# Optimization experiments

Measured on AMD Instinct MI355X. Metric: run time of the kernel, lower is better.

## Reference

```python
import jax, jax.numpy as jnp
import numpy as np

# Module constants (from init_kwargs)
X_RANGE = (-10.0, 10.0)
Y_RANGE = (-10.0, 10.0)
N_X = 64
N_Y = 64
B = 16
N_CTX = 1024


def make_grid():
    # x counted forward, y counted backwards (image-row convention):
    # grid[k*N_X + j] = (xs[j], ys[k]) with ys from max to min.
    xs = jnp.linspace(X_RANGE[0], X_RANGE[1], N_X, dtype=jnp.float32)
    ys = jnp.linspace(Y_RANGE[1], Y_RANGE[0], N_Y, dtype=jnp.float32)
    gx, gy = jnp.meshgrid(xs, ys)          # each (N_Y, N_X)
    return jnp.stack([gx, gy], axis=-1).reshape(-1, 2)  # (G, 2)


def setup_inputs() -> dict:
    key = jax.random.key(0)
    k1, k2 = jax.random.split(key)
    X = jax.random.uniform(k1, (B, N_CTX, 2), dtype=jnp.float32,
                           minval=X_RANGE[0], maxval=X_RANGE[1])
    Y = jax.random.normal(k2, (B, N_CTX, 2), dtype=jnp.float32)
    log_l_scale = jnp.zeros((), dtype=jnp.float32)  # log(1.0)
    return {"X": X, "Y": Y, "log_l_scale": log_l_scale}


def reference(X, Y, log_l_scale):
    grid = make_grid()                                  # (G, 2)
    l = jnp.exp(log_l_scale)
    # squared distances via expansion to avoid a (B,G,n,2) intermediate
    g2 = jnp.sum(grid * grid, axis=-1)                  # (G,)
    x2 = jnp.sum(X * X, axis=-1)                        # (B, n)
    gx = jnp.einsum('gd,bnd->bgn', grid, X)             # (B, G, n)
    d2 = g2[None, :, None] + x2[:, None, :] - 2.0 * gx  # (B, G, n)
    Gram = jnp.exp(-0.5 * d2 / (l * l))                 # RBF kernel, B=1
    # expand Y with a leading ones (density) channel
    ones = jnp.ones(Y.shape[:2] + (1,), dtype=Y.dtype)
    EY = jnp.concatenate([ones, Y], axis=-1)            # (B, n, 3)
    FM = jnp.einsum('bgn,bnc->bgc', Gram, EY)           # (B, G, 3)
    dens = FM[..., 0:1]
    FM = jnp.concatenate([dens, FM[..., 1:] / dens], axis=-1)
    # (B, G, 3) -> (B, 3, N_Y, N_X)
    return FM.reshape(X.shape[0], N_Y, N_X, 3).transpose(0, 3, 1, 2)
```

## Files before the change

### kernel.cpp

```cpp
#include <hip/hip_runtime.h>
#include <hip/hip_bf16.h>
#include <math.h>


#define NB    16
#define NCTX  1024
#define NG    4096
#define NQ    4
#define NPQ   (NCTX / NQ)
#define CELLS 256

__global__ __launch_bounds__(1024, 1)
void ee_single(const float* __restrict__ X,
               const float* __restrict__ Y,
               const float* __restrict__ log_l_scale,
               float* __restrict__ out) {
    const int b    = blockIdx.x >> 4;
    const int tile = blockIdx.x & 15;
    const int tid  = threadIdx.x;
    const int c    = tid & 255;
    const int q    = tid >> 8;
    const int ix   = c & 63;
    const int iy   = tile * 4 + (c >> 6);

    const float step  = 20.0f / 63.0f;
    const float scale = -0.72134752044448170f * expf(-2.0f * log_l_scale[0]);
    const float gx = -10.0f + step * (float)ix;
    const float gy =  10.0f - step * (float)iy;

    const int n0 = __builtin_amdgcn_readfirstlane(q * NPQ);

    const float2* Xb = (const float2*)(X + (size_t)b * NCTX * 2);
    const float2* Yb = (const float2*)(Y + (size_t)b * NCTX * 2);

    float d = 0.0f, a1 = 0.0f, a2 = 0.0f;
#pragma unroll 8
    for (int i = 0; i < NPQ; ++i) {
        const float2 xv = Xb[n0 + i];
        const float2 yv = Yb[n0 + i];
        const float dx = gx - xv.x;
        const float dy = gy - xv.y;
        float d2 = dx * dx;
        d2 = fmaf(dy, dy, d2);
        const float w = exp2f(d2 * scale);
        d  += w;
        a1 = fmaf(w, yv.x, a1);
        a2 = fmaf(w, yv.y, a2);
    }

    __shared__ float red[(NQ - 1) * CELLS * 3];
    if (q > 0) {
        float* r = &red[((q - 1) * CELLS + c) * 3];
        r[0] = d; r[1] = a1; r[2] = a2;
    }
    __syncthreads();
    if (q == 0) {
#pragma unroll
        for (int k = 0; k < NQ - 1; ++k) {
            const float* r = &red[(k * CELLS + c) * 3];
            d  += r[0];
            a1 += r[1];
            a2 += r[2];
        }
        const int g = tile * 256 + c;
        const float inv = 1.0f / d;
        float* ob = out + (size_t)b * 3 * NG;
        ob[g]          = d;
        ob[NG + g]     = a1 * inv;
        ob[2 * NG + g] = a2 * inv;
    }
}

extern "C" void kernel_launch(void* const* d_in, const int* in_sizes, int n_in,
                              void* d_out, int out_size, void* d_ws, size_t ws_size,
                              hipStream_t stream) {
    const float* X    = (const float*)d_in[0];
    const float* Y    = (const float*)d_in[1];
    const float* logl = (const float*)d_in[2];
    float* out = (float*)d_out;

    ee_single<<<dim3(NB * 16), dim3(1024), 0, stream>>>(X, Y, logl, out);
}
```

Baseline: 85.33 us.

## Stage context points in LDS and compute four grid rows per thread

Loads each batch's X and Y into shared memory as packed float4 once per block instead of having every thread read them from global memory. Each thread now covers one grid column across four rows, reusing the x-distance term and each loaded context point four times, and the context is split across 16 wavefronts of 64 points each. A larger 16-way shared-memory reduction then combines the partial sums. This cuts global and L1 traffic and per-point overhead, at the cost of more registers and a bigger reduction stage.

Measured after the change: 79.09 us. 7.3% less time.

```diff
diff --git a/kernel.cpp b/kernel.cpp
--- a/kernel.cpp
+++ b/kernel.cpp
@@ -6,68 +6,81 @@
 #define NB    16
 #define NCTX  1024
 #define NG    4096
-#define NQ    4
-#define NPQ   (NCTX / NQ)
-#define CELLS 256
+#define NW    16
+#define NPW   64
 
 __global__ __launch_bounds__(1024, 1)
-void ee_single(const float* __restrict__ X,
-               const float* __restrict__ Y,
-               const float* __restrict__ log_l_scale,
-               float* __restrict__ out) {
+void ee_single2(const float* __restrict__ X,
+                const float* __restrict__ Y,
+                const float* __restrict__ log_l_scale,
+                float* __restrict__ out) {
     const int b    = blockIdx.x >> 4;
     const int tile = blockIdx.x & 15;
     const int tid  = threadIdx.x;
-    const int c    = tid & 255;
-    const int q    = tid >> 8;
-    const int ix   = c & 63;
-    const int iy   = tile * 4 + (c >> 6);
+    const int q    = tid >> 6;
+    const int l    = tid & 63;
 
     const float step  = 20.0f / 63.0f;
     const float scale = -0.72134752044448170f * expf(-2.0f * log_l_scale[0]);
-    const float gx = -10.0f + step * (float)ix;
-    const float gy =  10.0f - step * (float)iy;
+    const float gx = -10.0f + step * (float)l;
+    float gy[4];
+#pragma unroll
+    for (int k = 0; k < 4; ++k)
+        gy[k] = 10.0f - step * (float)(tile * 4 + k);
 
-    const int n0 = __builtin_amdgcn_readfirstlane(q * NPQ);
+    __shared__ float4 sxy[NCTX];
+    __shared__ float  red[NW][3][256];
+    {
+        const float2* Xb = (const float2*)(X + (size_t)b * NCTX * 2);
+        const float2* Yb = (const float2*)(Y + (size_t)b * NCTX * 2);
+        const float2 xv = Xb[tid];
+        const float2 yv = Yb[tid];
+        sxy[tid] = make_float4(xv.x, xv.y, yv.x, yv.y);
+    }
+    __syncthreads();
 
-    const float2* Xb = (const float2*)(X + (size_t)b * NCTX * 2);
-    const float2* Yb = (const float2*)(Y + (size_t)b * NCTX * 2);
-
-    float d = 0.0f, a1 = 0.0f, a2 = 0.0f;
-#pragma unroll 8
-    for (int i = 0; i < NPQ; ++i) {
-        const float2 xv = Xb[n0 + i];
-        const float2 yv = Yb[n0 + i];
-        const float dx = gx - xv.x;
-        const float dy = gy - xv.y;
-        float d2 = dx * dx;
-        d2 = fmaf(dy, dy, d2);
-        const float w = exp2f(d2 * scale);
-        d  += w;
-        a1 = fmaf(w, yv.x, a1);
-        a2 = fmaf(w, yv.y, a2);
+    float d[4] = {0, 0, 0, 0}, a1[4] = {0, 0, 0, 0}, a2[4] = {0, 0, 0, 0};
+    const int n0 = q * NPW;
+#pragma unroll 4
+    for (int i = 0; i < NPW; ++i) {
+        const float4 v = sxy[n0 + i];
+        const float dx = gx - v.x;
+        const float tb = (dx * dx) * scale;
+#pragma unroll
+        for (int k = 0; k < 4; ++k) {
+            const float dy = gy[k] - v.y;
+            const float t  = fmaf(dy * scale, dy, tb);
+            const float w  = exp2f(t);
+            d[k]  += w;
+            a1[k]  = fmaf(w, v.z, a1[k]);
+            a2[k]  = fmaf(w, v.w, a2[k]);
+        }
     }
 
-    __shared__ float red[(NQ - 1) * CELLS * 3];
-    if (q > 0) {
-        float* r = &red[((q - 1) * CELLS + c) * 3];
-        r[0] = d; r[1] = a1; r[2] = a2;
+#pragma unroll
+    for (int k = 0; k < 4; ++k) {
+        const int c = k * 64 + l;
+        red[q][0][c] = d[k];
+        red[q][1][c] = a1[k];
+        red[q][2][c] = a2[k];
     }
     __syncthreads();
-    if (q == 0) {
+
+    if (tid < 256) {
+        const int c = tid;
+        float r0 = 0, r1 = 0, r2 = 0;
 #pragma unroll
-        for (int k = 0; k < NQ - 1; ++k) {
-            const float* r = &red[(k * CELLS + c) * 3];
-            d  += r[0];
-            a1 += r[1];
-            a2 += r[2];
+        for (int k = 0; k < NW; ++k) {
+            r0 += red[k][0][c];
+            r1 += red[k][1][c];
+            r2 += red[k][2][c];
         }
         const int g = tile * 256 + c;
-        const float inv = 1.0f / d;
+        const float inv = 1.0f / r0;
         float* ob = out + (size_t)b * 3 * NG;
-        ob[g]          = d;
-        ob[NG + g]     = a1 * inv;
-        ob[2 * NG + g] = a2 * inv;
+        ob[g]          = r0;
+        ob[NG + g]     = r1 * inv;
+        ob[2 * NG + g] = r2 * inv;
     }
 }
 
@@ -79,5 +92,5 @@
     const float* logl = (const float*)d_in[2];
     float* out = (float*)d_out;
 
-    ee_single<<<dim3(NB * 16), dim3(1024), 0, stream>>>(X, Y, logl, out);
+    ee_single2<<<dim3(256), dim3(1024), 0, stream>>>(X, Y, logl, out);
 }
```
